# Performance work log

Hardware: AMD Instinct MI355X
Metric: run time of the kernel (lower is better)

The kernel has to match this reference:

```python
import jax, jax.numpy as jnp
import numpy as np

B, H, W = 8, 1080, 1920


def setup_inputs() -> dict:
    key = jax.random.key(0)
    k1, k2 = jax.random.split(key)
    flow = jax.random.normal(k1, (B, 2, H, W), jnp.float32) * 10.0  # ~10px motion
    depth = jax.random.uniform(k2, (B, 1, H, W), jnp.float32) + 0.1  # positive weight
    return {"flow": flow, "depth": depth}


def _splat_avg(flow, depth):
    """Depth-weighted forward splat of -flow to the 4 integer pixels around the
    projected location (x+fx, y+fy), accumulate a weight buffer, then average."""
    Bn, _, Hn, Wn = flow.shape
    fx, fy = flow[:, 0], flow[:, 1]                 # [B,H,W]
    col = jnp.arange(Wn, dtype=flow.dtype)
    row = jnp.arange(Hn, dtype=flow.dtype)[:, None]
    x2 = col + fx
    y2 = row + fy
    valid = (x2 >= 0) & (x2 <= Wn - 1) & (y2 >= 0) & (y2 <= Hn - 1)
    ixL = jnp.clip(jnp.floor(x2).astype(jnp.int32), 0, Wn - 1)
    iyT = jnp.clip(jnp.floor(y2).astype(jnp.int32), 0, Hn - 1)
    ixR = jnp.minimum(ixL + 1, Wn - 1)
    iyB = jnp.minimum(iyT + 1, Hn - 1)
    w = jnp.where(valid, depth[:, 0], 0.0)          # depth weight, 0 if off-frame
    b_off = (jnp.arange(Bn, dtype=jnp.int32) * (Hn * Wn))[:, None, None]
    corners = [(iyT, ixL), (iyT, ixR), (iyB, ixL), (iyB, ixR)]
    lin = jnp.stack([b_off + iy * Wn + ix for iy, ix in corners]).reshape(-1)  # [4*B*H*W]
    vals = jnp.stack([-fx * w, -fy * w, w])         # [3,B,H,W]
    vals = jnp.broadcast_to(vals[:, None], (3, 4, Bn, Hn, Wn)).reshape(3, -1)
    acc = jnp.zeros((3, Bn * Hn * Wn), flow.dtype).at[:, lin].add(vals)
    out = acc[:2].reshape(2, Bn, Hn, Wn).transpose(1, 0, 2, 3)   # [B,2,H,W]
    count = acc[2].reshape(Bn, 1, Hn, Wn)                        # [B,1,H,W]
    denom = jnp.where(count > 0, count, 1.0)
    out = out / denom                                            # avg pass
    return out, count


def _fillhole(out, count):
    """For hole pixels (count==0), average the nearest filled pixel found in
    each of the 4 axis directions (left/right/up/down), equal weights."""
    mask = count[:, 0] > 0                           # [B,H,W]
    Bn, Hn, Wn = mask.shape
    col = jnp.arange(Wn, dtype=jnp.int32)
    row = jnp.arange(Hn, dtype=jnp.int32)[:, None]

    a = jnp.where(mask, col, -1)
    incl = jax.lax.associative_scan(jnp.maximum, a, axis=2)
    left = jnp.pad(incl[:, :, :-1], ((0, 0), (0, 0), (1, 0)), constant_values=-1)
    a = jnp.where(mask, col, Wn)
    incl = jax.lax.associative_scan(jnp.minimum, a, axis=2, reverse=True)
    right = jnp.pad(incl[:, :, 1:], ((0, 0), (0, 0), (0, 1)), constant_values=Wn)
    a = jnp.where(mask, row, -1)
    incl = jax.lax.associative_scan(jnp.maximum, a, axis=1)
    up = jnp.pad(incl[:, :-1, :], ((0, 0), (1, 0), (0, 0)), constant_values=-1)
    a = jnp.where(mask, row, Hn)
    incl = jax.lax.associative_scan(jnp.minimum, a, axis=1, reverse=True)
    down = jnp.pad(incl[:, 1:, :], ((0, 0), (0, 1), (0, 0)), constant_values=Hn)

    def gather(idx, axis, bound):
        found = ((idx >= 0) & (idx < bound))[:, None]        # [B,1,H,W]
        ic = jnp.clip(idx, 0, bound - 1)[:, None]
        v = jnp.take_along_axis(out, jnp.broadcast_to(ic, out.shape), axis=axis)
        return v, found.astype(out.dtype)

    vl, wl = gather(left, 3, Wn)
    vr, wr = gather(right, 3, Wn)
    vu, wu = gather(up, 2, Hn)
    vd, wd = gather(down, 2, Hn)
    s = wl + wr + wu + wd
    fill = (wl * vl + wr * vr + wu * vu + wd * vd) / jnp.maximum(s, 1.0)
    hole = (~mask)[:, None]
    return jnp.where(hole & (s > 0), fill, out)


def reference(flow, depth):
    out, count = _splat_avg(flow, depth)
    out = _fillhole(out, count)   # torch module runs fillhole when requires_grad=False
    return out
```

## Files before the change

kernel.cpp:

```cpp
#include <hip/hip_runtime.h>

#define BB 8
#define HH 1080
#define WW 1920
constexpr int HWc  = HH * WW;
constexpr int Ntot = BB * HWc;

constexpr int TILE = 64;
constexpr int MAR  = 32;
constexpr int REG  = TILE + 2 * MAR;
constexpr int WT   = WW / TILE;
constexpr int HT   = (HH + TILE - 1) / TILE;
constexpr int NTILE = WT * HT;
constexpr int GT    = NTILE * BB;
constexpr int CAP   = 256;

constexpr int SDIM = 65;
constexpr int SSTR = 66;
constexpr int PL   = SSTR * SSTR;

static_assert(TILE == 64, "ownership test uses >>6");
static_assert((WW & 3) == 0 && (HWc & 3) == 0, "float4 groups must not straddle");
static_assert(3 * PL * 4 <= 53000, "need 3 blocks/CU");


__global__ __launch_bounds__(256) void prepass_k(const float* __restrict__ flow,
                                                 const float* __restrict__ depth,
                                                 unsigned* __restrict__ cnt,
                                                 float4* __restrict__ buckets) {
    constexpr int NG = Ntot / 4;
    int g = blockIdx.x * 256 + threadIdx.x;
    if (g >= NG) return;
    int idx = g << 2;
    int b = idx / HWc;
    int p = idx - b * HWc;
    int y = p / WW;
    int x = p - y * WW;

    const size_t fbase = (size_t)b * 2 * HWc;
    float4 fx4 = *(const float4*)(flow + fbase + p);
    float4 fy4 = *(const float4*)(flow + fbase + HWc + p);

    float m = fmaxf(fmaxf(fmaxf(fabsf(fx4.x), fabsf(fx4.y)),
                          fmaxf(fabsf(fx4.z), fabsf(fx4.w))),
                    fmaxf(fmaxf(fabsf(fy4.x), fabsf(fy4.y)),
                          fmaxf(fabsf(fy4.z), fabsf(fy4.w))));
    if (m <= 30.f) return;

    const float fxs[4] = {fx4.x, fx4.y, fx4.z, fx4.w};
    const float fys[4] = {fy4.x, fy4.y, fy4.z, fy4.w};

#pragma unroll
    for (int c = 0; c < 4; ++c) {
        float fx = fxs[c], fy = fys[c];
        int xs = x + c;
        float x2 = (float)xs + fx;
        float y2 = (float)y + fy;
        if (!(x2 >= 0.f && x2 <= (float)(WW - 1) && y2 >= 0.f && y2 <= (float)(HH - 1)))
            continue;
        int ixL = (int)floorf(x2);
        int iyT = (int)floorf(y2);
        int ixR = min(ixL + 1, WW - 1);
        int iyB = min(iyT + 1, HH - 1);
        int cxs[2] = {ixL, ixR};
        int cys[2] = {iyT, iyB};
        bool anyOut = false;
#pragma unroll
        for (int a = 0; a < 2; ++a)
#pragma unroll
            for (int cc = 0; cc < 2; ++cc) {
                int cx = cxs[cc], cy = cys[a];
                int ox = (cx >> 6) * TILE - MAR;
                int oy = (cy >> 6) * TILE - MAR;
                if (!(xs >= ox && xs < ox + REG && y >= oy && y < oy + REG))
                    anyOut = true;
            }
        if (!anyOut) continue;

        float w = depth[(size_t)b * HWc + p + c];
        float vx = -fx * w;
        float vy = -fy * w;
#pragma unroll
        for (int a = 0; a < 2; ++a)
#pragma unroll
            for (int cc = 0; cc < 2; ++cc) {
                int cx = cxs[cc], cy = cys[a];
                int ox = (cx >> 6) * TILE - MAR;
                int oy = (cy >> 6) * TILE - MAR;
                if (!(xs >= ox && xs < ox + REG && y >= oy && y < oy + REG)) {
                    int gtile = b * NTILE + (cy >> 6) * WT + (cx >> 6);
                    unsigned slot = atomicAdd(&cnt[gtile], 1u);
                    if (slot < (unsigned)CAP) {
                        float4 rec;
                        rec.x = __int_as_float(((cy & 63) << 6) | (cx & 63));
                        rec.y = vx; rec.z = vy; rec.w = w;
                        buckets[(size_t)gtile * CAP + slot] = rec;
                    }
                }
            }
    }
}

#define PROC(FXC, FYC, DWC, CGX)                                               \
    {                                                                          \
        float fx = (FXC), fy = (FYC);                                          \
        float x2 = (float)(CGX) + fx, y2 = gyf + fy;                           \
        if (x2 >= 0.f && x2 <= (float)(WW - 1) &&                              \
            y2 >= 0.f && y2 <= (float)(HH - 1)) {                              \
            int ixL = (int)floorf(x2);        \
            int iyT = (int)floorf(y2);                                         \
            unsigned cI = (unsigned)(ixL - (X0 - 1));                          \
            unsigned rI = (unsigned)(iyT - (Y0 - 1));                          \
            if (cI < (unsigned)SDIM && rI < (unsigned)SDIM) {                  \
                float w = (DWC);                                               \
                if (ixL == WW - 1) w += w;      \
                if (iyT == HH - 1) w += w;      \
                int cell = (int)(rI * SSTR + cI);                              \
                atomicAdd(&sm[cell],          -fx * w);                        \
                atomicAdd(&sm[cell + PL],     -fy * w);                        \
                atomicAdd(&sm[cell + 2 * PL], w);                              \
            }                                                                  \
        }                                                                      \
    }

__global__ __launch_bounds__(512, 6) void tile_k(const float* __restrict__ flow,
                                                 const float* __restrict__ depth,
                                                 const unsigned* __restrict__ cnt,
                                                 const float4* __restrict__ buckets,
                                                 float* __restrict__ out,
                                                 unsigned char* __restrict__ mask) {
    __shared__ float sm[3 * PL];
    const int bid  = blockIdx.x;
    const int b    = bid & 7;
    const int tile = bid >> 3;
    const int ty   = tile / WT;
    const int tx   = tile - ty * WT;
    const int X0 = tx * TILE, Y0 = ty * TILE;
    const int rx0 = X0 - MAR, ry0 = Y0 - MAR;
    const int tid = threadIdx.x;

    float4* sm4 = (float4*)sm;
    for (int i = tid; i < 3 * PL / 4; i += 512)
        sm4[i] = make_float4(0.f, 0.f, 0.f, 0.f);
    __syncthreads();

    const float* fxp = flow + (size_t)b * 2 * HWc;
    const float* fyp = fxp + HWc;
    const float* dp  = depth + (size_t)b * HWc;

    const int gx  = rx0 + ((tid & 31) << 2);
    const bool xok = (unsigned)gx < (unsigned)WW;
    int gy = ry0 + (tid >> 5);
    float4 cfx, cfy, cd;
    bool ok = xok && ((unsigned)gy < (unsigned)HH);
    if (ok) {
        int p = gy * WW + gx;
        cfx = *(const float4*)(fxp + p);
        cfy = *(const float4*)(fyp + p);
        cd  = *(const float4*)(dp + p);
    }
#pragma unroll
    for (int k = 0; k < 8; ++k) {
        float4 nfx, nfy, nd;
        bool nok = false;
        const int ngy = gy + 16;
        if (k < 7) {
            nok = xok && ((unsigned)ngy < (unsigned)HH);
            if (nok) {
                int np = ngy * WW + gx;
                nfx = *(const float4*)(fxp + np);
                nfy = *(const float4*)(fyp + np);
                nd  = *(const float4*)(dp + np);
            }
        }
        if (ok) {
            const float gyf = (float)gy;
            PROC(cfx.x, cfy.x, cd.x, gx)
            PROC(cfx.y, cfy.y, cd.y, gx + 1)
            PROC(cfx.z, cfy.z, cd.z, gx + 2)
            PROC(cfx.w, cfy.w, cd.w, gx + 3)
        }
        ok = nok; gy = ngy; cfx = nfx; cfy = nfy; cd = nd;
    }
    __syncthreads();

    const int gtile = b * NTILE + tile;
    unsigned nrec = cnt[gtile];
    if (nrec > (unsigned)CAP) nrec = CAP;
    const float4* bkt = buckets + (size_t)gtile * CAP;

    float* o0 = out + (size_t)b * 2 * HWc;
    float* o1 = o0 + HWc;
    unsigned char* mb = mask + (size_t)b * HWc;
#pragma unroll
    for (int k = 0; k < 2; ++k) {
        int j   = k * 512 + tid;
        int row = j >> 4;
        int gy2 = Y0 + row;
        if (gy2 < HH) {
            int c0 = (j & 15) << 2;
            int q  = gy2 * WW + X0 + c0;
            const int rA = (row + 1) * SSTR + c0;
            const int rB = row * SSTR + c0;
            float4 vx, vy, wv;
            {
                float a_0 = sm[rA], a_1 = sm[rA+1], a_2 = sm[rA+2], a_3 = sm[rA+3], a_4 = sm[rA+4];
                float b_0 = sm[rB], b_1 = sm[rB+1], b_2 = sm[rB+2], b_3 = sm[rB+3], b_4 = sm[rB+4];
                vx.x = a_0+a_1+b_0+b_1; vx.y = a_1+a_2+b_1+b_2;
                vx.z = a_2+a_3+b_2+b_3; vx.w = a_3+a_4+b_3+b_4;
            }
            {
                const int oA = rA + PL, oB = rB + PL;
                float a_0 = sm[oA], a_1 = sm[oA+1], a_2 = sm[oA+2], a_3 = sm[oA+3], a_4 = sm[oA+4];
                float b_0 = sm[oB], b_1 = sm[oB+1], b_2 = sm[oB+2], b_3 = sm[oB+3], b_4 = sm[oB+4];
                vy.x = a_0+a_1+b_0+b_1; vy.y = a_1+a_2+b_1+b_2;
                vy.z = a_2+a_3+b_2+b_3; vy.w = a_3+a_4+b_3+b_4;
            }
            {
                const int oA = rA + 2 * PL, oB = rB + 2 * PL;
                float a_0 = sm[oA], a_1 = sm[oA+1], a_2 = sm[oA+2], a_3 = sm[oA+3], a_4 = sm[oA+4];
                float b_0 = sm[oB], b_1 = sm[oB+1], b_2 = sm[oB+2], b_3 = sm[oB+3], b_4 = sm[oB+4];
                wv.x = a_0+a_1+b_0+b_1; wv.y = a_1+a_2+b_1+b_2;
                wv.z = a_2+a_3+b_2+b_3; wv.w = a_3+a_4+b_3+b_4;
            }
            for (unsigned r = 0; r < nrec; ++r) {
                float4 rec = bkt[r];
                int cc = __float_as_int(rec.x);
                if ((cc >> 2) == j) {
                    switch (cc & 3) {
                    case 0: vx.x += rec.y; vy.x += rec.z; wv.x += rec.w; break;
                    case 1: vx.y += rec.y; vy.y += rec.z; wv.y += rec.w; break;
                    case 2: vx.z += rec.y; vy.z += rec.z; wv.z += rec.w; break;
                    default: vx.w += rec.y; vy.w += rec.z; wv.w += rec.w; break;
                    }
                }
            }
            float i0 = wv.x > 0.f ? 1.f / wv.x : 0.f;
            float i1 = wv.y > 0.f ? 1.f / wv.y : 0.f;
            float i2 = wv.z > 0.f ? 1.f / wv.z : 0.f;
            float i3 = wv.w > 0.f ? 1.f / wv.w : 0.f;
            float4 r0, r1;
            r0.x = vx.x * i0; r0.y = vx.y * i1; r0.z = vx.z * i2; r0.w = vx.w * i3;
            r1.x = vy.x * i0; r1.y = vy.y * i1; r1.z = vy.z * i2; r1.w = vy.w * i3;
            *(float4*)(o0 + q) = r0;
            *(float4*)(o1 + q) = r1;
            uchar4 mk;
            mk.x = (unsigned char)(wv.x > 0.f);
            mk.y = (unsigned char)(wv.y > 0.f);
            mk.z = (unsigned char)(wv.z > 0.f);
            mk.w = (unsigned char)(wv.w > 0.f);
            *(uchar4*)(mb + q) = mk;
        }
    }
}

__global__ __launch_bounds__(256) void fill_k(float* __restrict__ out,
                                              const unsigned char* __restrict__ mask) {
    constexpr int NG = Ntot / 4;
    int g = blockIdx.x * 256 + threadIdx.x;
    if (g >= NG) return;
    int idx0 = g << 2;
    uchar4 m4 = *(const uchar4*)(mask + idx0);
    if (m4.x & m4.y & m4.z & m4.w) return;

    int b = idx0 / HWc;
    int p0 = idx0 - b * HWc;
    int y = p0 / WW;
    int x0 = p0 - y * WW;

    const unsigned char* mb = mask + (size_t)b * HWc;
    const float* o0 = out + (size_t)b * 2 * HWc;
    const float* o1 = o0 + HWc;
    const unsigned char ms[4] = {m4.x, m4.y, m4.z, m4.w};

#pragma unroll
    for (int c = 0; c < 4; ++c) {
        if (ms[c]) continue;
        int x = x0 + c;
        int p = p0 + c;
        float s = 0.f, s0 = 0.f, s1 = 0.f;
        for (int j = x - 1; j >= 0; --j) {
            if (mb[y * WW + j]) { int q = y * WW + j; s += 1.f; s0 += o0[q]; s1 += o1[q]; break; }
        }
        for (int j = x + 1; j < WW; ++j) {
            if (mb[y * WW + j]) { int q = y * WW + j; s += 1.f; s0 += o0[q]; s1 += o1[q]; break; }
        }
        for (int i = y - 1; i >= 0; --i) {
            if (mb[i * WW + x]) { int q = i * WW + x; s += 1.f; s0 += o0[q]; s1 += o1[q]; break; }
        }
        for (int i = y + 1; i < HH; ++i) {
            if (mb[i * WW + x]) { int q = i * WW + x; s += 1.f; s0 += o0[q]; s1 += o1[q]; break; }
        }
        if (s > 0.f) {
            ((float*)o0)[p] = s0 / s;
            ((float*)o1)[p] = s1 / s;
        }
    }
}

extern "C" void kernel_launch(void* const* d_in, const int* in_sizes, int n_in,
                              void* d_out, int out_size, void* d_ws, size_t ws_size,
                              hipStream_t stream) {
    const float* flow  = (const float*)d_in[0];
    const float* depth = (const float*)d_in[1];
    float* out = (float*)d_out;

    unsigned char* wsb = (unsigned char*)d_ws;
    unsigned* cnt      = (unsigned*)wsb;
    float4*  buckets   = (float4*)(wsb + 16384);
    unsigned char* mask = wsb + 16384 + (size_t)GT * CAP * 16;

    const int threads = 256;

    hipMemsetAsync(cnt, 0, (size_t)GT * sizeof(unsigned), stream);

    prepass_k<<<(Ntot / 4 + threads - 1) / threads, threads, 0, stream>>>(
        flow, depth, cnt, buckets);

    tile_k<<<GT, 512, 0, stream>>>(flow, depth, cnt, buckets, out, mask);

    fill_k<<<(Ntot / 4 + threads - 1) / threads, threads, 0, stream>>>(out, mask);
}
```

Before: 637.8 us.

## Fold spill prepass into tile kernel and apply spills in a separate fixup pass

Removes the standalone prepass that reread flow to bucket far-moving splats. Core pixels inside tile_k now append out-of-region contributions to buckets directly. A new fixup kernel accumulates those buckets in shared memory per tile and merges them into the already-normalized output, using a stored weight plane. This saves a full read of flow and the per-pixel bucket scan in tile_k, at the cost of writing an extra weight plane and launching an extra kernel. It also adds global atomics inside the hot splat loop.

```diff
diff --git a/kernel.cpp b/kernel.cpp
--- a/kernel.cpp
+++ b/kernel.cpp
@@ -23,82 +23,37 @@
 static_assert((WW & 3) == 0 && (HWc & 3) == 0, "float4 groups must not straddle");
 static_assert(3 * PL * 4 <= 53000, "need 3 blocks/CU");
 
-
-__global__ __launch_bounds__(256) void prepass_k(const float* __restrict__ flow,
-                                                 const float* __restrict__ depth,
-                                                 unsigned* __restrict__ cnt,
-                                                 float4* __restrict__ buckets) {
-    constexpr int NG = Ntot / 4;
-    int g = blockIdx.x * 256 + threadIdx.x;
-    if (g >= NG) return;
-    int idx = g << 2;
-    int b = idx / HWc;
-    int p = idx - b * HWc;
-    int y = p / WW;
-    int x = p - y * WW;
-
-    const size_t fbase = (size_t)b * 2 * HWc;
-    float4 fx4 = *(const float4*)(flow + fbase + p);
-    float4 fy4 = *(const float4*)(flow + fbase + HWc + p);
-
-    float m = fmaxf(fmaxf(fmaxf(fabsf(fx4.x), fabsf(fx4.y)),
-                          fmaxf(fabsf(fx4.z), fabsf(fx4.w))),
-                    fmaxf(fmaxf(fabsf(fy4.x), fabsf(fy4.y)),
-                          fmaxf(fabsf(fy4.z), fabsf(fy4.w))));
-    if (m <= 30.f) return;
-
-    const float fxs[4] = {fx4.x, fx4.y, fx4.z, fx4.w};
-    const float fys[4] = {fy4.x, fy4.y, fy4.z, fy4.w};
-
-#pragma unroll
-    for (int c = 0; c < 4; ++c) {
-        float fx = fxs[c], fy = fys[c];
-        int xs = x + c;
-        float x2 = (float)xs + fx;
-        float y2 = (float)y + fy;
-        if (!(x2 >= 0.f && x2 <= (float)(WW - 1) && y2 >= 0.f && y2 <= (float)(HH - 1)))
-            continue;
-        int ixL = (int)floorf(x2);
-        int iyT = (int)floorf(y2);
-        int ixR = min(ixL + 1, WW - 1);
-        int iyB = min(iyT + 1, HH - 1);
-        int cxs[2] = {ixL, ixR};
-        int cys[2] = {iyT, iyB};
-        bool anyOut = false;
-#pragma unroll
-        for (int a = 0; a < 2; ++a)
-#pragma unroll
-            for (int cc = 0; cc < 2; ++cc) {
-                int cx = cxs[cc], cy = cys[a];
-                int ox = (cx >> 6) * TILE - MAR;
-                int oy = (cy >> 6) * TILE - MAR;
-                if (!(xs >= ox && xs < ox + REG && y >= oy && y < oy + REG))
-                    anyOut = true;
-            }
-        if (!anyOut) continue;
-
-        float w = depth[(size_t)b * HWc + p + c];
-        float vx = -fx * w;
-        float vy = -fy * w;
-#pragma unroll
-        for (int a = 0; a < 2; ++a)
-#pragma unroll
-            for (int cc = 0; cc < 2; ++cc) {
-                int cx = cxs[cc], cy = cys[a];
-                int ox = (cx >> 6) * TILE - MAR;
-                int oy = (cy >> 6) * TILE - MAR;
-                if (!(xs >= ox && xs < ox + REG && y >= oy && y < oy + REG)) {
-                    int gtile = b * NTILE + (cy >> 6) * WT + (cx >> 6);
-                    unsigned slot = atomicAdd(&cnt[gtile], 1u);
-                    if (slot < (unsigned)CAP) {
-                        float4 rec;
-                        rec.x = __int_as_float(((cy & 63) << 6) | (cx & 63));
-                        rec.y = vx; rec.z = vy; rec.w = w;
-                        buckets[(size_t)gtile * CAP + slot] = rec;
-                    }
+constexpr size_t OFF_BKT  = 16384;
+constexpr size_t OFF_MASK = OFF_BKT + (size_t)GT * CAP * 16;
+constexpr size_t OFF_W    = OFF_MASK + (size_t)Ntot;
+static_assert(OFF_W % 16 == 0, "wplane must be float4-aligned");
+
+__device__ inline void spill_append(int b, int xs, int ys, int ixL, int iyT,
+                                    float fx, float fy, float w,
+                                    unsigned* cnt, float4* buckets) {
+    int ixR = min(ixL + 1, WW - 1);
+    int iyB = min(iyT + 1, HH - 1);
+    int cxs[2] = {ixL, ixR};
+    int cys[2] = {iyT, iyB};
+    float vx = -fx * w, vy = -fy * w;
+#pragma unroll
+    for (int a = 0; a < 2; ++a)
+#pragma unroll
+        for (int cc = 0; cc < 2; ++cc) {
+            int cx = cxs[cc], cy = cys[a];
+            int ox = (cx >> 6) * TILE - MAR;
+            int oy = (cy >> 6) * TILE - MAR;
+            if (!(xs >= ox && xs < ox + REG && ys >= oy && ys < oy + REG)) {
+                int gtile = b * NTILE + (cy >> 6) * WT + (cx >> 6);
+                unsigned slot = atomicAdd(&cnt[gtile], 1u);
+                if (slot < (unsigned)CAP) {
+                    float4 rec;
+                    rec.x = __int_as_float(((cy & 63) << 6) | (cx & 63));
+                    rec.y = vx; rec.z = vy; rec.w = w;
+                    buckets[(size_t)gtile * CAP + slot] = rec;
                 }
             }
-    }
+        }
 }
 
 #define PROC(FXC, FYC, DWC, CGX)                                               \
@@ -120,15 +75,19 @@
                 atomicAdd(&sm[cell + PL],     -fy * w);                        \
                 atomicAdd(&sm[cell + 2 * PL], w);                              \
             }                                                                  \
+            if (core && (fabsf(fx) > 30.f || fabsf(fy) > 30.f))                \
+                spill_append(b, (CGX), gy, ixL, iyT, fx, fy, (DWC),            \
+                             cnt, buckets);                                    \
         }                                                                      \
     }
 
 __global__ __launch_bounds__(512, 6) void tile_k(const float* __restrict__ flow,
                                                  const float* __restrict__ depth,
-                                                 const unsigned* __restrict__ cnt,
-                                                 const float4* __restrict__ buckets,
+                                                 unsigned* __restrict__ cnt,
+                                                 float4* __restrict__ buckets,
                                                  float* __restrict__ out,
-                                                 unsigned char* __restrict__ mask) {
+                                                 unsigned char* __restrict__ mask,
+                                                 float* __restrict__ wplane) {
     __shared__ float sm[3 * PL];
     const int bid  = blockIdx.x;
     const int b    = bid & 7;
@@ -150,6 +109,7 @@
 
     const int gx  = rx0 + ((tid & 31) << 2);
     const bool xok = (unsigned)gx < (unsigned)WW;
+    const bool xin = (unsigned)(gx - X0) < (unsigned)TILE;
     int gy = ry0 + (tid >> 5);
     float4 cfx, cfy, cd;
     bool ok = xok && ((unsigned)gy < (unsigned)HH);
@@ -175,6 +135,7 @@
         }
         if (ok) {
             const float gyf = (float)gy;
+            const bool core = xin && ((unsigned)(gy - Y0) < (unsigned)TILE);
             PROC(cfx.x, cfy.x, cd.x, gx)
             PROC(cfx.y, cfy.y, cd.y, gx + 1)
             PROC(cfx.z, cfy.z, cd.z, gx + 2)
@@ -184,13 +145,9 @@
     }
     __syncthreads();
 
-    const int gtile = b * NTILE + tile;
-    unsigned nrec = cnt[gtile];
-    if (nrec > (unsigned)CAP) nrec = CAP;
-    const float4* bkt = buckets + (size_t)gtile * CAP;
-
     float* o0 = out + (size_t)b * 2 * HWc;
     float* o1 = o0 + HWc;
+    float* wp = wplane + (size_t)b * HWc;
     unsigned char* mb = mask + (size_t)b * HWc;
 #pragma unroll
     for (int k = 0; k < 2; ++k) {
@@ -223,18 +180,6 @@
                 wv.x = a_0+a_1+b_0+b_1; wv.y = a_1+a_2+b_1+b_2;
                 wv.z = a_2+a_3+b_2+b_3; wv.w = a_3+a_4+b_3+b_4;
             }
-            for (unsigned r = 0; r < nrec; ++r) {
-                float4 rec = bkt[r];
-                int cc = __float_as_int(rec.x);
-                if ((cc >> 2) == j) {
-                    switch (cc & 3) {
-                    case 0: vx.x += rec.y; vy.x += rec.z; wv.x += rec.w; break;
-                    case 1: vx.y += rec.y; vy.y += rec.z; wv.y += rec.w; break;
-                    case 2: vx.z += rec.y; vy.z += rec.z; wv.z += rec.w; break;
-                    default: vx.w += rec.y; vy.w += rec.z; wv.w += rec.w; break;
-                    }
-                }
-            }
             float i0 = wv.x > 0.f ? 1.f / wv.x : 0.f;
             float i1 = wv.y > 0.f ? 1.f / wv.y : 0.f;
             float i2 = wv.z > 0.f ? 1.f / wv.z : 0.f;
@@ -244,12 +189,66 @@
             r1.x = vy.x * i0; r1.y = vy.y * i1; r1.z = vy.z * i2; r1.w = vy.w * i3;
             *(float4*)(o0 + q) = r0;
             *(float4*)(o1 + q) = r1;
+            *(float4*)(wp + q) = wv;
             uchar4 mk;
             mk.x = (unsigned char)(wv.x > 0.f);
             mk.y = (unsigned char)(wv.y > 0.f);
             mk.z = (unsigned char)(wv.z > 0.f);
             mk.w = (unsigned char)(wv.w > 0.f);
             *(uchar4*)(mb + q) = mk;
+        }
+    }
+}
+
+__global__ __launch_bounds__(256) void fixup_k(const unsigned* __restrict__ cnt,
+                                               const float4* __restrict__ buckets,
+                                               float* __restrict__ out,
+                                               const float* __restrict__ wplane,
+                                               unsigned char* __restrict__ mask) {
+    __shared__ float s[3 * 4096];
+    int gtile = blockIdx.x;
+    unsigned n = cnt[gtile];
+    if (n == 0) return;
+    if (n > (unsigned)CAP) n = CAP;
+    int b  = gtile / NTILE;
+    int t  = gtile - b * NTILE;
+    int ty = t / WT, tx = t - ty * WT;
+    int X0 = tx * TILE, Y0 = ty * TILE;
+
+    float4* s4 = (float4*)s;
+    for (int i = threadIdx.x; i < 3 * 4096 / 4; i += 256)
+        s4[i] = make_float4(0.f, 0.f, 0.f, 0.f);
+    __syncthreads();
+
+    const float4* bkt = buckets + (size_t)gtile * CAP;
+    for (unsigned r = threadIdx.x; r < n; r += 256) {
+        float4 rec = bkt[r];
+        int cell = __float_as_int(rec.x);
+        atomicAdd(&s[cell],        rec.y);
+        atomicAdd(&s[cell + 4096], rec.z);
+        atomicAdd(&s[cell + 8192], rec.w);
+    }
+    __syncthreads();
+
+    float* o0 = out + (size_t)b * 2 * HWc;
+    float* o1 = o0 + HWc;
+    const float* wp = wplane + (size_t)b * HWc;
+    unsigned char* mb = mask + (size_t)b * HWc;
+    for (int cell = threadIdx.x; cell < 4096; cell += 256) {
+        float ws = s[cell + 8192];
+        if (ws != 0.f) {
+            int cy = Y0 + (cell >> 6), cx = X0 + (cell & 63);
+            if (cy < HH) {
+                int q = cy * WW + cx;
+                float w0 = wp[q];
+                float wn = w0 + ws;
+                float v0 = o0[q] * w0 + s[cell];
+                float v1 = o1[q] * w0 + s[cell + 4096];
+                float inv = wn > 0.f ? 1.f / wn : 0.f;
+                o0[q] = v0 * inv;
+                o1[q] = v1 * inv;
+                mb[q] = 1;
+            }
         }
     }
 }
@@ -306,18 +305,18 @@
     float* out = (float*)d_out;
 
     unsigned char* wsb = (unsigned char*)d_ws;
-    unsigned* cnt      = (unsigned*)wsb;
-    float4*  buckets   = (float4*)(wsb + 16384);
-    unsigned char* mask = wsb + 16384 + (size_t)GT * CAP * 16;
+    unsigned* cnt       = (unsigned*)wsb;
+    float4*  buckets    = (float4*)(wsb + OFF_BKT);
+    unsigned char* mask = wsb + OFF_MASK;
+    float*   wplane     = (float*)(wsb + OFF_W);
 
     const int threads = 256;
 
     hipMemsetAsync(cnt, 0, (size_t)GT * sizeof(unsigned), stream);
 
-    prepass_k<<<(Ntot / 4 + threads - 1) / threads, threads, 0, stream>>>(
-        flow, depth, cnt, buckets);
-
-    tile_k<<<GT, 512, 0, stream>>>(flow, depth, cnt, buckets, out, mask);
+    tile_k<<<GT, 512, 0, stream>>>(flow, depth, cnt, buckets, out, mask, wplane);
+
+    fixup_k<<<GT, threads, 0, stream>>>(cnt, buckets, out, wplane, mask);
 
     fill_k<<<(Ntot / 4 + threads - 1) / threads, threads, 0, stream>>>(out, mask);
 }
```

New measurement: 606.9 us. 1.05x faster.
